# Kernel optimization log

Hardware: AMD Instinct MI355X
Metric: run time of the kernel (lower is better)

Reference implementation:

```python
import jax, jax.numpy as jnp
import numpy as np

T, B, I, H = 512, 64, 1024, 1024


def setup_inputs() -> dict:
    key = jax.random.key(0)
    ks = jax.random.split(key, 9)
    g_x = 1.0 / np.sqrt(I)   # glorot-ish scale
    g_h = 1.0 / np.sqrt(H)
    return {
        "X": jax.random.normal(ks[0], (T, B, I), dtype=jnp.float32),
        "Wa_x": jax.random.normal(ks[1], (I, H), dtype=jnp.float32) * g_x,
        "Wi_x": jax.random.normal(ks[2], (I, H), dtype=jnp.float32) * g_x,
        "Wf_x": jax.random.normal(ks[3], (I, H), dtype=jnp.float32) * g_x,
        "Wo_x": jax.random.normal(ks[4], (I, H), dtype=jnp.float32) * g_x,
        "Wa_h": jax.random.normal(ks[5], (H, H), dtype=jnp.float32) * g_h,
        "Wi_h": jax.random.normal(ks[6], (H, H), dtype=jnp.float32) * g_h,
        "Wf_h": jax.random.normal(ks[7], (H, H), dtype=jnp.float32) * g_h,
        "Wo_h": jax.random.normal(ks[8], (H, H), dtype=jnp.float32) * g_h,
        "ba": jnp.zeros((H,), dtype=jnp.float32),
        "bi": jnp.zeros((H,), dtype=jnp.float32),
        "bf": jnp.zeros((H,), dtype=jnp.float32),
        "bo": jnp.zeros((H,), dtype=jnp.float32),
    }


def reference(X, Wa_x, Wi_x, Wf_x, Wo_x, Wa_h, Wi_h, Wf_h, Wo_h, ba, bi, bf, bo):
    # Fuse the 4 input-to-gate GEMMs across all timesteps (no recurrence there):
    # Xg: [T, B, 4H] with gate order (a, i, f, o)
    Wx = jnp.concatenate([Wa_x, Wi_x, Wf_x, Wo_x], axis=1)  # [I, 4H]
    Wh = jnp.concatenate([Wa_h, Wi_h, Wf_h, Wo_h], axis=1)  # [H, 4H]
    b = jnp.concatenate([ba, bi, bf, bo], axis=0)           # [4H]
    Xg = jnp.einsum("tbi,ig->tbg", X, Wx) + b               # [T, B, 4H]

    Hd = Wa_h.shape[0]

    def step(carry, xg):
        h, s = carry
        g = xg + h @ Wh  # [B, 4H]; at t=0, h=0 so matches the t==0 branch
        a = jnp.tanh(g[:, 0 * Hd:1 * Hd])
        i = jax.nn.sigmoid(g[:, 1 * Hd:2 * Hd])
        f = jax.nn.sigmoid(g[:, 2 * Hd:3 * Hd])
        o = jax.nn.sigmoid(g[:, 3 * Hd:4 * Hd])
        s_new = a * i + s * f
        h_new = jnp.tanh(s_new) * o
        return (h_new, s_new), h_new

    Bsz = X.shape[1]
    init = (jnp.zeros((Bsz, Hd), X.dtype), jnp.zeros((Bsz, Hd), X.dtype))
    _, outputs = jax.lax.scan(step, init, Xg)  # [T, B, H]
    return outputs


if __name__ == "__main__":
    out = reference(**setup_inputs())
    print(out.shape)
```

## Files before the change

kernel.cpp:

```cpp
#include <hip/hip_runtime.h>
#include <hip/hip_bf16.h>

typedef __bf16 bf8 __attribute__((ext_vector_type(8)));
typedef float  f32x4 __attribute__((ext_vector_type(4)));
typedef unsigned long long u64;

#define TT 512
#define BBATCH 64
#define IDIM 1024
#define HDIM 1024
#define G4 4096
#define NREC 128

__device__ __forceinline__ float sigf(float x) {
  x = fminf(fmaxf(x, -30.f), 30.f);
  return 1.f / (1.f + __expf(-x));
}
__device__ __forceinline__ float tanh_(float x) {
  x = fminf(fmaxf(x, -15.f), 15.f);
  float e = __expf(2.f * x);
  return (e - 1.f) / (e + 1.f);
}
__device__ __forceinline__ f32x4 MFMA(bf8 a, bf8 b, f32x4 c) {
  return __builtin_amdgcn_mfma_f32_16x16x32_bf16(a, b, c, 0, 0, 0);
}

__global__ __launch_bounds__(256) void k_convw(
    const float* __restrict__ s0, const float* __restrict__ s1,
    const float* __restrict__ s2, const float* __restrict__ s3,
    const float* __restrict__ s4, const float* __restrict__ s5,
    const float* __restrict__ s6, const float* __restrict__ s7,
    __bf16* __restrict__ WxT, __bf16* __restrict__ WhT) {
  int z = blockIdx.z;
  const float* src = (z == 0) ? s0 : (z == 1) ? s1 : (z == 2) ? s2 :
                     (z == 3) ? s3 : (z == 4) ? s4 : (z == 5) ? s5 :
                     (z == 6) ? s6 : s7;
  __bf16* dst = (z < 4) ? WxT : WhT;
  int j0 = blockIdx.x * 64, k0 = blockIdx.y * 64;
  __shared__ float T[64][65];
  int tid = threadIdx.x;
#pragma unroll
  for (int i = 0; i < 16; ++i) {
    int idx = tid + i * 256;
    int kl = idx >> 6, jl = idx & 63;
    T[kl][jl] = src[(size_t)(k0 + kl) * 1024 + j0 + jl];
  }
  __syncthreads();
#pragma unroll
  for (int i = 0; i < 2; ++i) {
    int Gt = tid + i * 256;
    int nl = Gt >> 3, gq = Gt & 7;
    int n = (z & 3) * 1024 + j0 + nl;
    bf8 v;
#pragma unroll
    for (int e = 0; e < 8; ++e) v[e] = (__bf16)T[gq * 8 + e][nl];
    *(bf8*)&dst[(size_t)n * 1024 + k0 + gq * 8] = v;
  }
}

__global__ void k_bias(const float* __restrict__ b0, const float* __restrict__ b1,
                       const float* __restrict__ b2, const float* __restrict__ b3,
                       float* __restrict__ bias) {
  int i = blockIdx.x * 256 + threadIdx.x;
  if (i < G4) {
    const float* s = (i < 1024) ? b0 : (i < 2048) ? b1 : (i < 3072) ? b2 : b3;
    bias[i] = s[i & 1023];
  }
}

__global__ __launch_bounds__(512, 2) void k_fused(
    const float* __restrict__ Xg_r, float* __restrict__ Xg_w,
    const __bf16* __restrict__ WhT, const __bf16* __restrict__ WxT,
    const float* __restrict__ Xnext, const float* __restrict__ bias,
    __bf16* __restrict__ hb0, __bf16* __restrict__ hb1,
    float* __restrict__ S, float* __restrict__ out,
    int* flags, int t0, int Tc, int nrec, int gM) {
  __shared__ char smem[65536];
  const int bid = blockIdx.x, tid = threadIdx.x;
  const int lane = tid & 63, w = tid >> 6;

  if (bid < nrec) {
    bf8 (*Ls)[128] = (bf8(*)[128])smem;
    float* Gsf = (float*)smem;
    const int ct = w & 3, kh = w >> 2;
    const int rh = bid & 1, hc0 = (bid >> 1) * 16;
    const int l15 = lane & 15, lq = lane >> 4;
    const int rowbase = rh * 32;

    bf8 Bf[16];
#pragma unroll
    for (int s = 0; s < 16; ++s)
      Bf[s] = *(const bf8*)&WhT[(size_t)(ct * 1024 + hc0 + l15) * 1024 +
                                kh * 512 + s * 32 + lq * 8];
#pragma unroll
    for (int i = 0; i < 16; ++i) {
      float4 tpin = __builtin_bit_cast(float4, Bf[i]);
      asm volatile("" : "+v"(tpin.x), "+v"(tpin.y), "+v"(tpin.z), "+v"(tpin.w));
      Bf[i] = __builtin_bit_cast(bf8, tpin);
    }

    const int er = tid >> 4, ec = tid & 15;
    float sreg = 0.f;
    if (t0 > 0) sreg = S[(size_t)(rowbase + er) * 1024 + hc0 + ec];

    for (int lt = 0; lt < Tc; ++lt) {
      const int t = t0 + lt;

      const float* xp = Xg_r + ((size_t)lt * 64 + rowbase + er) * G4 + hc0 + ec;
      float xa = xp[0], xi = xp[1024], xf = xp[2048], xo = xp[3072];

      f32x4 acc0 = {}, acc1 = {};

      if (t > 0) {
        if (lt > 0) {
          int v;
          do {
            v = __hip_atomic_load(flags + (2 * lane + rh) * 32, __ATOMIC_RELAXED,
                                  __HIP_MEMORY_SCOPE_AGENT);
          } while (!__all(v >= t));
          asm volatile("" ::: "memory");
        }
        const __bf16* hp = ((t - 1) & 1) ? hb1 : hb0;

        union { u64 q[2]; bf8 v; } vv[8];
#pragma unroll
        for (int i = 0; i < 8; ++i) {
          int g = i * 512 + tid;
          const u64* sp = (const u64*)(hp + (size_t)(rowbase + (g >> 7)) * 1024 +
                                       (g & 127) * 8);
          vv[i].q[0] = __hip_atomic_load((u64*)sp, __ATOMIC_RELAXED,
                                         __HIP_MEMORY_SCOPE_AGENT);
          vv[i].q[1] = __hip_atomic_load((u64*)sp + 1, __ATOMIC_RELAXED,
                                         __HIP_MEMORY_SCOPE_AGENT);
        }
#pragma unroll
        for (int i = 0; i < 8; ++i) {
          int g = i * 512 + tid, r = g >> 7, cg = g & 127;
          Ls[r][cg ^ (r & 7)] = vv[i].v;
        }
        __syncthreads();

#pragma unroll
        for (int s = 0; s < 16; ++s) {
          int kk = kh * 64 + s * 4 + lq;
          bf8 af0 = Ls[l15][kk ^ (l15 & 7)];
          bf8 af1 = Ls[16 + l15][kk ^ (l15 & 7)];
          acc0 = MFMA(af0, Bf[s], acc0);
          acc1 = MFMA(af1, Bf[s], acc1);
        }
        __syncthreads();

        {
          float* G = Gsf + kh * 2176 + ct * 16 + l15;
#pragma unroll
          for (int q = 0; q < 4; ++q) {
            G[(lq * 4 + q) * 68]        = acc0[q];
            G[(16 + lq * 4 + q) * 68]   = acc1[q];
          }
        }
        __syncthreads();

        const float* Gr = Gsf + er * 68 + ec;
        xa += Gr[0]  + Gr[2176 + 0];
        xi += Gr[16] + Gr[2176 + 16];
        xf += Gr[32] + Gr[2176 + 32];
        xo += Gr[48] + Gr[2176 + 48];
      }

      float av = tanh_(xa), iv = sigf(xi), fv = sigf(xf), ov = sigf(xo);
      sreg = av * iv + sreg * fv;
      float h0 = tanh_(sreg) * ov;

      out[((size_t)t * 64 + rowbase + er) * 1024 + hc0 + ec] = h0;

      float hnb = __shfl(h0, lane + 1);
      if ((ec & 1) == 0) {
        unsigned int pv =
            (unsigned int)__builtin_bit_cast(unsigned short, (__bf16)h0) |
            ((unsigned int)__builtin_bit_cast(unsigned short, (__bf16)hnb) << 16);
        __bf16* hn = (t & 1) ? hb1 : hb0;
        __hip_atomic_store(
            (unsigned int*)((char*)hn + ((size_t)(rowbase + er) * 1024 + hc0 + ec) * 2),
            pv, __ATOMIC_RELAXED, __HIP_MEMORY_SCOPE_AGENT);
      }

      __syncthreads();
      if (tid == 0)
        __hip_atomic_store(flags + bid * 32, t + 1, __ATOMIC_RELAXED,
                           __HIP_MEMORY_SCOPE_AGENT);
    }

    S[(size_t)(rowbase + er) * 1024 + hc0 + ec] = sreg;
    return;
  }

  if (gM == 0) return;
  const int nw = gridDim.x - nrec;
  const int wid = bid - nrec;
  __bf16 (*As)[40] = (__bf16(*)[40])smem;
  __bf16 (*Bs)[40] = (__bf16(*)[40])(smem + 128 * 40 * 2);
  const int wr = (w >> 2) * 64, wc = (w & 3) * 32;
  const int sm = tid >> 2, sk = (tid & 3) * 8;
  const int gl15 = lane & 15, glq = lane >> 4;
  const int ntiles = (gM / 128) * (G4 / 128);

  for (int tile = wid; tile < ntiles; tile += nw) {
    const int m0 = (tile >> 5) * 128, n0 = (tile & 31) * 128;
    const float*  Ap = Xnext + (size_t)(m0 + sm) * 1024 + sk;
    const __bf16* Bp = WxT + (size_t)(n0 + sm) * 1024 + sk;
    f32x4 acc[4][2] = {};
    float4 ra0, ra1;
    bf8 rb;
    auto ld = [&](int kt) {
      ra0 = *(const float4*)(Ap + kt * 32);
      ra1 = *(const float4*)(Ap + kt * 32 + 4);
      rb = *(const bf8*)(Bp + kt * 32);
    };
    ld(0);
    for (int kt = 0; kt < 32; ++kt) {
      __syncthreads();
      bf8 va;
      va[0]=(__bf16)ra0.x; va[1]=(__bf16)ra0.y; va[2]=(__bf16)ra0.z; va[3]=(__bf16)ra0.w;
      va[4]=(__bf16)ra1.x; va[5]=(__bf16)ra1.y; va[6]=(__bf16)ra1.z; va[7]=(__bf16)ra1.w;
      *(bf8*)&As[sm][sk] = va;
      *(bf8*)&Bs[sm][sk] = rb;
      if (kt < 31) ld(kt + 1);
      __syncthreads();
      bf8 af[4], bv[2];
#pragma unroll
      for (int r = 0; r < 4; ++r) af[r] = *(const bf8*)&As[wr + r * 16 + gl15][glq * 8];
#pragma unroll
      for (int c = 0; c < 2; ++c) bv[c] = *(const bf8*)&Bs[wc + c * 16 + gl15][glq * 8];
#pragma unroll
      for (int r = 0; r < 4; ++r)
#pragma unroll
        for (int c = 0; c < 2; ++c)
          acc[r][c] = MFMA(af[r], bv[c], acc[r][c]);
    }
#pragma unroll
    for (int c = 0; c < 2; ++c) {
      int col = n0 + wc + c * 16 + gl15;
      float bc = bias[col];
#pragma unroll
      for (int r = 0; r < 4; ++r)
#pragma unroll
        for (int q = 0; q < 4; ++q)
          Xg_w[(size_t)(m0 + wr + r * 16 + glq * 4 + q) * G4 + col] = acc[r][c][q] + bc;
    }
    __syncthreads();
  }
}

extern "C" void kernel_launch(void* const* d_in, const int* in_sizes, int n_in,
                              void* d_out, int out_size, void* d_ws, size_t ws_size,
                              hipStream_t stream) {
  const float* X  = (const float*)d_in[0];
  const float* wa = (const float*)d_in[1];
  const float* wi = (const float*)d_in[2];
  const float* wf = (const float*)d_in[3];
  const float* wo = (const float*)d_in[4];
  const float* ha = (const float*)d_in[5];
  const float* hi = (const float*)d_in[6];
  const float* hf = (const float*)d_in[7];
  const float* ho = (const float*)d_in[8];
  const float* b0 = (const float*)d_in[9];
  const float* b1 = (const float*)d_in[10];
  const float* b2 = (const float*)d_in[11];
  const float* b3 = (const float*)d_in[12];
  float* out = (float*)d_out;
  char* ws = (char*)d_ws;

  size_t off = 0;
  auto alloc = [&](size_t bytes) {
    void* p = ws + off;
    off += (bytes + 255) & ~(size_t)255;
    return p;
  };
  __bf16* WxT = (__bf16*)alloc((size_t)G4 * IDIM * 2);
  __bf16* WhT = (__bf16*)alloc((size_t)G4 * HDIM * 2);
  float* bias = (float*)alloc(G4 * 4);
  float* S    = (float*)alloc((size_t)BBATCH * HDIM * 4);
  __bf16* hb0 = (__bf16*)alloc((size_t)BBATCH * HDIM * 2);
  __bf16* hb1 = (__bf16*)alloc((size_t)BBATCH * HDIM * 2);
  int* flags  = (int*)alloc(NREC * 32 * 4);
  size_t base = off;

  const size_t perXg = (size_t)BBATCH * G4 * 4;
  int Tc = 64;
  while (Tc > 4 && base + 2 * (size_t)Tc * perXg > ws_size) Tc >>= 1;
  float* Xg0 = (float*)(ws + base);
  float* Xg1 = (float*)(ws + base + (size_t)Tc * perXg);
  int nchunks = TT / Tc;

  k_convw<<<dim3(16, 16, 8), dim3(256), 0, stream>>>(wa, wi, wf, wo, ha, hi, hf,
                                                     ho, WxT, WhT);
  k_bias<<<dim3(16), dim3(256), 0, stream>>>(b0, b1, b2, b3, bias);
  hipMemsetAsync(flags, 0, NREC * 32 * 4, stream);

  k_fused<<<dim3(256), dim3(512), 0, stream>>>(
      nullptr, Xg0, WhT, WxT, X, bias, hb0, hb1, S, out, flags,
      0, 0, 0, Tc * BBATCH);

  for (int c = 0; c < nchunks; ++c) {
    float* xr = (c & 1) ? Xg1 : Xg0;
    float* xw = (c & 1) ? Xg0 : Xg1;
    int gM = (c + 1 < nchunks) ? Tc * BBATCH : 0;
    const float* Xn = X + (size_t)(c + 1) * Tc * BBATCH * IDIM;
    k_fused<<<dim3(256), dim3(512), 0, stream>>>(
        xr, xw, WhT, WxT, Xn, bias, hb0, hb1, S, out, flags,
        c * Tc, Tc, NREC, gM);
  }
}
```

Baseline: 2.227 ms.

## Split recurrent GEMM across K per wave and load h directly into registers

Each of the 8 waves now owns a 128-wide K slice covering all four gates, and loads its h fragments from global memory straight into MFMA operand registers instead of staging h through LDS. The partial sums from the 8 K-slices are written to a swizzled LDS buffer and reduced in a separate pass. This removes the LDS staging of h and one barrier from each serial timestep, at the cost of an 8-way cross-wave reduction and more accumulator registers. Launch bounds are lowered to one block per CU, giving the compiler more registers.

Result: slower. 3.044 ms (+36.7%).

```diff
diff --git a/kernel.cpp b/kernel.cpp
--- a/kernel.cpp
+++ b/kernel.cpp
@@ -68,7 +68,7 @@
   }
 }
 
-__global__ __launch_bounds__(512, 2) void k_fused(
+__global__ __launch_bounds__(512, 1) void k_fused(
     const float* __restrict__ Xg_r, float* __restrict__ Xg_w,
     const __bf16* __restrict__ WhT, const __bf16* __restrict__ WxT,
     const float* __restrict__ Xnext, const float* __restrict__ bias,
@@ -80,23 +80,24 @@
   const int lane = tid & 63, w = tid >> 6;
 
   if (bid < nrec) {
-    bf8 (*Ls)[128] = (bf8(*)[128])smem;
     float* Gsf = (float*)smem;
-    const int ct = w & 3, kh = w >> 2;
+    const int kq = w;
     const int rh = bid & 1, hc0 = (bid >> 1) * 16;
     const int l15 = lane & 15, lq = lane >> 4;
     const int rowbase = rh * 32;
 
     bf8 Bf[16];
 #pragma unroll
-    for (int s = 0; s < 16; ++s)
-      Bf[s] = *(const bf8*)&WhT[(size_t)(ct * 1024 + hc0 + l15) * 1024 +
-                                kh * 512 + s * 32 + lq * 8];
+    for (int g = 0; g < 4; ++g)
+#pragma unroll
+      for (int s = 0; s < 4; ++s)
+        Bf[g * 4 + s] = *(const bf8*)&WhT[(size_t)(g * 1024 + hc0 + l15) * 1024 +
+                                          kq * 128 + s * 32 + lq * 8];
 #pragma unroll
     for (int i = 0; i < 16; ++i) {
-      float4 tpin = __builtin_bit_cast(float4, Bf[i]);
-      asm volatile("" : "+v"(tpin.x), "+v"(tpin.y), "+v"(tpin.z), "+v"(tpin.w));
-      Bf[i] = __builtin_bit_cast(bf8, tpin);
+      float4 tp = __builtin_bit_cast(float4, Bf[i]);
+      asm volatile("" : "+v"(tp.x), "+v"(tp.y), "+v"(tp.z), "+v"(tp.w));
+      Bf[i] = __builtin_bit_cast(bf8, tp);
     }
 
     const int er = tid >> 4, ec = tid & 15;
@@ -108,8 +109,6 @@
 
       const float* xp = Xg_r + ((size_t)lt * 64 + rowbase + er) * G4 + hc0 + ec;
       float xa = xp[0], xi = xp[1024], xf = xp[2048], xo = xp[3072];
-
-      f32x4 acc0 = {}, acc1 = {};
 
       if (t > 0) {
         if (lt > 0) {
@@ -122,49 +121,62 @@
         }
         const __bf16* hp = ((t - 1) & 1) ? hb1 : hb0;
 
-        union { u64 q[2]; bf8 v; } vv[8];
-#pragma unroll
-        for (int i = 0; i < 8; ++i) {
-          int g = i * 512 + tid;
-          const u64* sp = (const u64*)(hp + (size_t)(rowbase + (g >> 7)) * 1024 +
-                                       (g & 127) * 8);
-          vv[i].q[0] = __hip_atomic_load((u64*)sp, __ATOMIC_RELAXED,
-                                         __HIP_MEMORY_SCOPE_AGENT);
-          vv[i].q[1] = __hip_atomic_load((u64*)sp + 1, __ATOMIC_RELAXED,
-                                         __HIP_MEMORY_SCOPE_AGENT);
-        }
-#pragma unroll
-        for (int i = 0; i < 8; ++i) {
-          int g = i * 512 + tid, r = g >> 7, cg = g & 127;
-          Ls[r][cg ^ (r & 7)] = vv[i].v;
-        }
-        __syncthreads();
-
-#pragma unroll
-        for (int s = 0; s < 16; ++s) {
-          int kk = kh * 64 + s * 4 + lq;
-          bf8 af0 = Ls[l15][kk ^ (l15 & 7)];
-          bf8 af1 = Ls[16 + l15][kk ^ (l15 & 7)];
-          acc0 = MFMA(af0, Bf[s], acc0);
-          acc1 = MFMA(af1, Bf[s], acc1);
-        }
-        __syncthreads();
-
-        {
-          float* G = Gsf + kh * 2176 + ct * 16 + l15;
-#pragma unroll
-          for (int q = 0; q < 4; ++q) {
-            G[(lq * 4 + q) * 68]        = acc0[q];
-            G[(16 + lq * 4 + q) * 68]   = acc1[q];
+        u64 aq[16];
+#pragma unroll
+        for (int mh = 0; mh < 2; ++mh) {
+          const __bf16* hr = hp + (size_t)(rowbase + mh * 16 + l15) * 1024 +
+                             kq * 128 + lq * 8;
+#pragma unroll
+          for (int s = 0; s < 4; ++s) {
+            const u64* p = (const u64*)(hr + s * 32);
+            aq[(mh * 4 + s) * 2 + 0] = __hip_atomic_load(p, __ATOMIC_RELAXED,
+                                                         __HIP_MEMORY_SCOPE_AGENT);
+            aq[(mh * 4 + s) * 2 + 1] = __hip_atomic_load(p + 1, __ATOMIC_RELAXED,
+                                                         __HIP_MEMORY_SCOPE_AGENT);
           }
         }
-        __syncthreads();
-
-        const float* Gr = Gsf + er * 68 + ec;
-        xa += Gr[0]  + Gr[2176 + 0];
-        xi += Gr[16] + Gr[2176 + 16];
-        xf += Gr[32] + Gr[2176 + 32];
-        xo += Gr[48] + Gr[2176 + 48];
+
+        f32x4 acc[2][4] = {};
+#pragma unroll
+        for (int s = 0; s < 4; ++s)
+#pragma unroll
+          for (int mh = 0; mh < 2; ++mh) {
+            union { u64 q[2]; bf8 v; } u;
+            u.q[0] = aq[(mh * 4 + s) * 2 + 0];
+            u.q[1] = aq[(mh * 4 + s) * 2 + 1];
+            acc[mh][0] = MFMA(u.v, Bf[0 * 4 + s], acc[mh][0]);
+            acc[mh][1] = MFMA(u.v, Bf[1 * 4 + s], acc[mh][1]);
+            acc[mh][2] = MFMA(u.v, Bf[2 * 4 + s], acc[mh][2]);
+            acc[mh][3] = MFMA(u.v, Bf[3 * 4 + s], acc[mh][3]);
+          }
+
+#pragma unroll
+        for (int mh = 0; mh < 2; ++mh)
+#pragma unroll
+          for (int g = 0; g < 4; ++g)
+            *(f32x4*)&Gsf[(size_t)((kq * 64 + g * 16 + l15) * 32 +
+                                   ((mh * 16 + lq * 4) ^ ((l15 & 7) << 2)))] =
+                acc[mh][g];
+      }
+      __syncthreads();
+
+      if (t > 0) {
+        const int ncl = tid >> 3;
+        const int r4 = ((tid & 7) * 4) ^ ((ncl & 7) << 2);
+        f32x4 sum = *(const f32x4*)&Gsf[(size_t)(ncl * 32 + r4)];
+#pragma unroll
+        for (int k2 = 1; k2 < 8; ++k2)
+          sum += *(const f32x4*)&Gsf[(size_t)((k2 * 64 + ncl) * 32 + r4)];
+        *(f32x4*)&Gsf[(size_t)(ncl * 32 + r4)] = sum;
+      }
+      __syncthreads();
+
+      if (t > 0) {
+        const int key = (ec & 7) << 2;
+        xa += Gsf[(0 * 16 + ec) * 32 + (er ^ key)];
+        xi += Gsf[(1 * 16 + ec) * 32 + (er ^ key)];
+        xf += Gsf[(2 * 16 + ec) * 32 + (er ^ key)];
+        xo += Gsf[(3 * 16 + ec) * 32 + (er ^ key)];
       }
 
       float av = tanh_(xa), iv = sigf(xi), fv = sigf(xf), ov = sigf(xo);
```

## Switch recurrent matmul to 32x32x16 MFMA with 4-way K split

Applied to the files above, without the earlier changes.

Replaces the per-wave pair of 16x16x32 MFMAs with a single 32x32x16 MFMA per k-step. The 8 waves are reorganized into 2 column groups by 4 K-quarters, and the partial sums are reduced through a swizzled LDS layout. The goal is fewer MFMA issues and A-fragment LDS reads on the latency-critical recurrent step. In exchange the cross-wave reduction is larger (four partials per output instead of two), and launch bounds drop to one block per CU, which changes register budget and occupancy.

After: 2.109 ms. 1.06x faster.

```diff
diff --git a/kernel.cpp b/kernel.cpp
--- a/kernel.cpp
+++ b/kernel.cpp
@@ -2,7 +2,8 @@
 #include <hip/hip_bf16.h>
 
 typedef __bf16 bf8 __attribute__((ext_vector_type(8)));
-typedef float  f32x4 __attribute__((ext_vector_type(4)));
+typedef float  f32x4  __attribute__((ext_vector_type(4)));
+typedef float  f32x16 __attribute__((ext_vector_type(16)));
 typedef unsigned long long u64;
 
 #define TT 512
@@ -23,6 +24,9 @@
 }
 __device__ __forceinline__ f32x4 MFMA(bf8 a, bf8 b, f32x4 c) {
   return __builtin_amdgcn_mfma_f32_16x16x32_bf16(a, b, c, 0, 0, 0);
+}
+__device__ __forceinline__ f32x16 MFMA32(bf8 a, bf8 b, f32x16 c) {
+  return __builtin_amdgcn_mfma_f32_32x32x16_bf16(a, b, c, 0, 0, 0);
 }
 
 __global__ __launch_bounds__(256) void k_convw(
@@ -68,7 +72,7 @@
   }
 }
 
-__global__ __launch_bounds__(512, 2) void k_fused(
+__global__ __launch_bounds__(512, 1) void k_fused(
     const float* __restrict__ Xg_r, float* __restrict__ Xg_w,
     const __bf16* __restrict__ WhT, const __bf16* __restrict__ WxT,
     const float* __restrict__ Xnext, const float* __restrict__ bias,
@@ -82,21 +86,24 @@
   if (bid < nrec) {
     bf8 (*Ls)[128] = (bf8(*)[128])smem;
     float* Gsf = (float*)smem;
-    const int ct = w & 3, kh = w >> 2;
+    const int nc = w & 1, kq = w >> 1;
     const int rh = bid & 1, hc0 = (bid >> 1) * 16;
-    const int l15 = lane & 15, lq = lane >> 4;
+    const int l31 = lane & 31, hi = lane >> 5;
     const int rowbase = rh * 32;
 
     bf8 Bf[16];
-#pragma unroll
-    for (int s = 0; s < 16; ++s)
-      Bf[s] = *(const bf8*)&WhT[(size_t)(ct * 1024 + hc0 + l15) * 1024 +
-                                kh * 512 + s * 32 + lq * 8];
+    {
+      const int lc = nc * 32 + l31;
+      const __bf16* wp = WhT + (size_t)((lc >> 4) * 1024 + hc0 + (lc & 15)) * 1024 +
+                         kq * 256 + hi * 8;
+#pragma unroll
+      for (int s = 0; s < 16; ++s) Bf[s] = *(const bf8*)(wp + s * 16);
+    }
 #pragma unroll
     for (int i = 0; i < 16; ++i) {
-      float4 tpin = __builtin_bit_cast(float4, Bf[i]);
-      asm volatile("" : "+v"(tpin.x), "+v"(tpin.y), "+v"(tpin.z), "+v"(tpin.w));
-      Bf[i] = __builtin_bit_cast(bf8, tpin);
+      float4 tp = __builtin_bit_cast(float4, Bf[i]);
+      asm volatile("" : "+v"(tp.x), "+v"(tp.y), "+v"(tp.z), "+v"(tp.w));
+      Bf[i] = __builtin_bit_cast(bf8, tp);
     }
 
     const int er = tid >> 4, ec = tid & 15;
@@ -108,8 +115,6 @@
 
       const float* xp = Xg_r + ((size_t)lt * 64 + rowbase + er) * G4 + hc0 + ec;
       float xa = xp[0], xi = xp[1024], xf = xp[2048], xo = xp[3072];
-
-      f32x4 acc0 = {}, acc1 = {};
 
       if (t > 0) {
         if (lt > 0) {
@@ -140,31 +145,42 @@
         }
         __syncthreads();
 
+        f32x16 acc = {};
 #pragma unroll
         for (int s = 0; s < 16; ++s) {
-          int kk = kh * 64 + s * 4 + lq;
-          bf8 af0 = Ls[l15][kk ^ (l15 & 7)];
-          bf8 af1 = Ls[16 + l15][kk ^ (l15 & 7)];
-          acc0 = MFMA(af0, Bf[s], acc0);
-          acc1 = MFMA(af1, Bf[s], acc1);
+          int c = (kq * 16 + s) * 2 + hi;
+          bf8 af = Ls[l31][c ^ (l31 & 7)];
+          acc = MFMA32(af, Bf[s], acc);
         }
         __syncthreads();
 
         {
-          float* G = Gsf + kh * 2176 + ct * 16 + l15;
+          float* gt = Gsf + (nc * 4 + kq) * 1024 + l31 * 32;
 #pragma unroll
           for (int q = 0; q < 4; ++q) {
-            G[(lq * 4 + q) * 68]        = acc0[q];
-            G[(16 + lq * 4 + q) * 68]   = acc1[q];
+            int rg = 2 * q + hi;
+            f32x4 v4 = { acc[4 * q + 0], acc[4 * q + 1],
+                         acc[4 * q + 2], acc[4 * q + 3] };
+            *(f32x4*)(gt + ((rg ^ (l31 & 7)) << 2)) = v4;
           }
         }
         __syncthreads();
 
-        const float* Gr = Gsf + er * 68 + ec;
-        xa += Gr[0]  + Gr[2176 + 0];
-        xi += Gr[16] + Gr[2176 + 16];
-        xf += Gr[32] + Gr[2176 + 32];
-        xo += Gr[48] + Gr[2176 + 48];
+        {
+          const int rg = er >> 2, e = er & 3;
+#pragma unroll
+          for (int g = 0; g < 4; ++g) {
+            int lc2 = g * 16 + ec;
+            int ncl = lc2 >> 5, col = lc2 & 31;
+            const float* gp = Gsf + ncl * 4096 + col * 32 +
+                              ((rg ^ (col & 7)) << 2) + e;
+            float v = gp[0] + gp[1024] + gp[2048] + gp[3072];
+            if (g == 0) xa += v;
+            else if (g == 1) xi += v;
+            else if (g == 2) xf += v;
+            else xo += v;
+          }
+        }
       }
 
       float av = tanh_(xa), iv = sigf(xi), fv = sigf(xf), ov = sigf(xo);
```
